# Optimization experiments

Measured on AMD Instinct MI355X. Metric: run time of the kernel, lower is better.

The kernel has to match this reference:

```python
import jax, jax.numpy as jnp
import numpy as np

N_HEAD = 16
T_THRESHOLD = 0.001


def setup_inputs() -> dict:
    key = jax.random.key(0)
    k_x, k_wa, k_ba, k_wp, k_bp = jax.random.split(key, 5)
    B, P, L, R = 8, 1024, 4, 256
    C = L * R  # n_embd = 1024
    s = 1.0 / np.sqrt(C)
    return {
        "x": jax.random.normal(k_x, (B, P, L, R), dtype=jnp.float32),
        "w_attn": jax.random.normal(k_wa, (C, 3 * C), dtype=jnp.float32) * s,
        "b_attn": jax.random.normal(k_ba, (3 * C,), dtype=jnp.float32) * 0.01,
        "w_proj": jax.random.normal(k_wp, (C, C), dtype=jnp.float32) * s,
        "b_proj": jax.random.normal(k_bp, (C,), dtype=jnp.float32) * 0.01,
    }


def reference(x, w_attn, b_attn, w_proj, b_proj):
    B, P, L, R = x.shape
    C = L * R
    H = N_HEAD
    hd = C // H
    xf = x.reshape(B, P, C)                      # (B, T, C)
    qkv = xf @ w_attn + b_attn                   # (B, T, 3C)
    q, k, v = jnp.split(qkv, 3, axis=-1)
    # (B, H, T, hd)
    q = q.reshape(B, P, H, hd).transpose(0, 2, 1, 3)
    k = k.reshape(B, P, H, hd).transpose(0, 2, 1, 3)
    v = v.reshape(B, P, H, hd).transpose(0, 2, 1, 3)
    att = jnp.einsum("bhqd,bhkd->bhqk", q, k) * (1.0 / np.sqrt(hd))
    att = jax.nn.softmax(att, axis=-1)
    att = jax.nn.relu(att - T_THRESHOLD)         # post-softmax thresholding
    y = jnp.einsum("bhqk,bhkd->bhqd", att, v)    # (B, H, T, hd)
    y = y.transpose(0, 2, 1, 3).reshape(B, P, C)
    y = y @ w_proj + b_proj
    return y.reshape(B, P, L, R)
```

## Files before the change

### kernel.cpp

```cpp
#include <hip/hip_runtime.h>


typedef _Float16 half8 __attribute__((ext_vector_type(8)));
typedef _Float16 half4_t __attribute__((ext_vector_type(4)));
typedef float floatx4 __attribute__((ext_vector_type(4)));

__device__ __forceinline__ void gl2lds16(const void* gsrc, void* lds) {
    __builtin_amdgcn_global_load_lds(
        (const __attribute__((address_space(1))) unsigned int*)gsrc,
        (__attribute__((address_space(3))) unsigned int*)lds,
        16, 0, 0);
}

__global__ __launch_bounds__(256) void prep(const float4* __restrict__ x4,
                                            _Float16* __restrict__ xh,
                                            const float* __restrict__ wa,
                                            _Float16* __restrict__ waT,
                                            const float* __restrict__ wp,
                                            _Float16* __restrict__ wpT) {
    __shared__ _Float16 t[64 * 65];
    int bid = blockIdx.x;
    if (bid < 4096) {
        int idx = bid * 256 + threadIdx.x;
#pragma unroll
        for (int i = idx; i < 2097152; i += 1048576) {
            float4 v = x4[i];
            half4_t h = { (_Float16)v.x, (_Float16)v.y, (_Float16)v.z, (_Float16)v.w };
            *(half4_t*)(xh + (size_t)i * 4) = h;
        }
    } else {
        int tt = bid - 4096;
        int by = tt & 15, bx = tt >> 4;
        const float* in = wa; _Float16* out = waT; int C = 3072;
        if (bx >= 48) { bx -= 48; in = wp; out = wpT; C = 1024; }
#pragma unroll
        for (int it = 0; it < 16; ++it) {
            int idx = it * 256 + threadIdx.x;
            int r = idx >> 6, c = idx & 63;
            t[c * 65 + r] = (_Float16)in[(size_t)(by * 64 + r) * C + bx * 64 + c];
        }
        __syncthreads();
#pragma unroll
        for (int it = 0; it < 16; ++it) {
            int idx = it * 256 + threadIdx.x;
            int rn = idx >> 6, ck = idx & 63;
            out[(size_t)(bx * 64 + rn) * 1024 + by * 64 + ck] = t[rn * 65 + ck];
        }
    }
}

#define GBAR __builtin_amdgcn_s_barrier()
#define WLGKM do { asm volatile("s_waitcnt lgkmcnt(0)" ::: "memory"); } while (0)
#define WVM2  do { asm volatile("s_waitcnt vmcnt(2)"   ::: "memory"); } while (0)
#define WVM4  do { asm volatile("s_waitcnt vmcnt(4)"   ::: "memory"); } while (0)
#define WVM0  do { asm volatile("s_waitcnt vmcnt(0)"   ::: "memory"); } while (0)


#define WLDA(buf, rg)                                                                         \
    do {                                                                                      \
        _Pragma("unroll") for (int i = 0; i < 4; ++i) {                                       \
            int r_ = wm * 128 + ((rg) * 4 + i) * 16 + l15;                                    \
            _Pragma("unroll") for (int kk = 0; kk < 2; ++kk)                                  \
                a[i][kk] = *(const half8*)(sA + (buf) * 32768 + r_ * 128 +                    \
                                           ((((kk << 2) + quad) ^ (r_ & 7)) << 4));           \
        }                                                                                     \
    } while (0)

#define WLDB(buf, cg, bb)                                                                     \
    do {                                                                                      \
        _Pragma("unroll") for (int j = 0; j < 2; ++j) {                                       \
            int r_ = wn * 64 + ((cg) * 2 + j) * 16 + l15;                                     \
            _Pragma("unroll") for (int kk = 0; kk < 2; ++kk)                                  \
                bb[j][kk] = *(const half8*)(sB + (buf) * 32768 + r_ * 128 +                   \
                                            ((((kk << 2) + quad) ^ (r_ & 7)) << 4));          \
        }                                                                                     \
    } while (0)

#define WMMA(rg, cg, bb)                                                                      \
    do {                                                                                      \
        __builtin_amdgcn_s_setprio(1);                                                        \
        _Pragma("unroll") for (int kk = 0; kk < 2; ++kk)                                      \
            _Pragma("unroll") for (int i = 0; i < 4; ++i)                                     \
                _Pragma("unroll") for (int j = 0; j < 2; ++j)                                  \
                    acc[(rg) * 4 + i][(cg) * 2 + j] = __builtin_amdgcn_mfma_f32_16x16x32_f16( \
                        a[i][kk], bb[j][kk], acc[(rg) * 4 + i][(cg) * 2 + j], 0, 0, 0);       \
        __builtin_amdgcn_s_setprio(0);                                                        \
    } while (0)

__global__ __launch_bounds__(512, 2) void gemm_qkv(const _Float16* __restrict__ A,
                                                   const _Float16* __restrict__ BT,
                                                   const float* __restrict__ bias,
                                                   _Float16* __restrict__ qno,
                                                   _Float16* __restrict__ kPo,
                                                   _Float16* __restrict__ vPo) {
    __shared__ __attribute__((aligned(16))) char lds[131072];
    char* sA = lds;
    char* sB = lds + 65536;
    int tid = threadIdx.x;
    int W = tid >> 6, lane = tid & 63, quad = lane >> 4, l15 = lane & 15;
    int wm = W >> 2, wn = W & 3;
    int flat = blockIdx.y * 12 + blockIdx.x;
    int swz = (flat & 7) * 48 + (flat >> 3);
    int m0 = (swz / 12) * 256, n0 = (swz % 12) * 256;

    auto stA = [&](int buf, int half, int k0) {
#pragma unroll
        for (int rnd = 0; rnd < 2; ++rnd) {
            int c = rnd * 512 + tid;
            int row = c >> 3;
            int q = (c & 7) ^ (row & 7);
            const _Float16* src = A + (size_t)(m0 + half * 128 + row) * 1024 + k0 + q * 8;
            int off = __builtin_amdgcn_readfirstlane(buf * 32768 + half * 16384 +
                                                     rnd * 8192 + (W << 10));
            gl2lds16(src, sA + off);
        }
    };
    auto stB = [&](int buf, int half, int k0) {
#pragma unroll
        for (int rnd = 0; rnd < 2; ++rnd) {
            int c = rnd * 512 + tid;
            int row = c >> 3;
            int q = (c & 7) ^ (row & 7);
            const _Float16* src = BT + (size_t)(n0 + half * 128 + row) * 1024 + k0 + q * 8;
            int off = __builtin_amdgcn_readfirstlane(buf * 32768 + half * 16384 +
                                                     rnd * 8192 + (W << 10));
            gl2lds16(src, sB + off);
        }
    };

    half8 a[4][2], b0[2][2], b1[2][2];
    floatx4 acc[8][4] = {};

    stA(0, 0, 0); stA(0, 1, 0);
    stB(0, 0, 0); stB(0, 1, 0);
    stB(1, 0, 64); stB(1, 1, 64);
    WVM4;
    GBAR;

#pragma unroll 1
    for (int t = 0; t < 16; t += 2) {
        int k1 = (t + 1) << 6;
        int k2 = ((t + 2) & 15) << 6;
        int k3 = ((t + 3) & 15) << 6;
        WLDA(0, 0); WLDB(0, 0, b0); stA(1, 0, k1);
        GBAR; WLGKM; WMMA(0, 0, b0); GBAR;
        WLDB(0, 1, b1); stA(1, 1, k1);
        GBAR; WLGKM; WMMA(0, 1, b1); GBAR;
        WLDA(0, 1); stB(0, 0, k2);
        GBAR; WLGKM; WMMA(1, 1, b1); GBAR;
        stB(0, 1, k2); WVM4;
        GBAR; WLGKM; WMMA(1, 0, b0); GBAR;
        WLDA(1, 0); WLDB(1, 0, b0); stA(0, 0, k2);
        GBAR; WLGKM; WMMA(0, 0, b0); GBAR;
        WLDB(1, 1, b1); stA(0, 1, k2);
        GBAR; WLGKM; WMMA(0, 1, b1); GBAR;
        WLDA(1, 1); stB(1, 0, k3);
        GBAR; WLGKM; WMMA(1, 1, b1); GBAR;
        stB(1, 1, k3); WVM4;
        GBAR; WLGKM; WMMA(1, 0, b0); GBAR;
    }

    WVM0;
    GBAR;
    int sec = n0 >> 10;
    int b = m0 >> 10;
    int tb = m0 & 1023;
#pragma unroll 1
    for (int p = 0; p < 2; ++p) {
        if (p) __syncthreads();
        if (sec == 2) {
            if ((wn >> 1) == p) {
#pragma unroll
                for (int cf = 0; cf < 4; ++cf) {
                    int lc = (wn & 1) * 64 + cf * 16 + l15;
                    float bv = bias[n0 + wn * 64 + cf * 16 + l15];
#pragma unroll
                    for (int rf = 0; rf < 8; ++rf) {
                        int m = wm * 128 + rf * 16 + quad * 4;
                        half4_t h4;
#pragma unroll
                        for (int r = 0; r < 4; ++r) h4[r] = (_Float16)(acc[rf][cf][r] + bv);
                        *(half4_t*)(lds + lc * 528 + m * 2) = h4;
                    }
                }
            }
            __syncthreads();
            int l15v = tid & 15;
            int moct = W * 4 + ((tid >> 4) & 3);
            int t = tb + moct * 8;
            int kbv = (t >> 5) & 31, quad_v = (t >> 3) & 3;
            int nbV = (n0 & 1023) + p * 128;
#pragma unroll
            for (int i = 0; i < 8; ++i) {
                int hh = i >> 2, cf = i & 3;
                int n = hh * 64 + cf * 16 + l15v;
                half8 v = *(const half8*)(lds + n * 528 + (moct << 4));
                int gcol = nbV + n;
                int h = gcol >> 6, d = gcol & 63;
                size_t chunk = (size_t)((b * 16 + h) * 32 + kbv) * 256 +
                               (d >> 4) * 64 + quad_v * 16 + (d & 15);
                *(half8*)(vPo + chunk * 8) = v;
            }
        } else {
            if ((wn >> 1) == p) {
#pragma unroll
                for (int cf = 0; cf < 4; ++cf) {
                    int lc = (wn & 1) * 64 + cf * 16 + l15;
                    float bv = bias[n0 + wn * 64 + cf * 16 + l15];
#pragma unroll
                    for (int rf = 0; rf < 8; ++rf) {
                        int m = wm * 128 + rf * 16 + quad * 4;
#pragma unroll
                        for (int r = 0; r < 4; ++r)
                            *(_Float16*)(lds + (m + r) * 272 + lc * 2) =
                                (_Float16)(acc[rf][cf][r] + bv);
                    }
                }
            }
            __syncthreads();
            int nb = (n0 & 1023) + p * 128;
            if (sec == 0) {
                int noct = tid & 15;
#pragma unroll
                for (int i = 0; i < 8; ++i) {
                    int m = i * 32 + (tid >> 4);
                    half8 v = *(const half8*)(lds + m * 272 + (noct << 4));
                    *(half8*)(qno + (size_t)(b * 1024 + tb + m) * 1024 + nb + noct * 8) = v;
                }
            } else {
                int l15k = tid & 15, noct = (tid >> 4) & 15;
#pragma unroll
                for (int i = 0; i < 8; ++i) {
                    int mb = i * 2 + (tid >> 8);
                    int m = mb * 16 + l15k;
                    half8 v = *(const half8*)(lds + m * 272 + (noct << 4));
                    int gcol = nb + noct * 8;
                    int h = gcol >> 6, d0 = gcol & 63;
                    int t = tb + m;
                    size_t chunk = (size_t)((b * 16 + h) * 64 + (t >> 4)) * 128 +
                                   (d0 >> 5) * 64 + ((d0 >> 3) & 3) * 16 + l15k;
                    *(half8*)(kPo + chunk * 8) = v;
                }
            }
        }
    }
}

#define LDA(buf, rg)                                                                          \
    do {                                                                                      \
        _Pragma("unroll") for (int i = 0; i < 2; ++i) {                                       \
            int r_ = wm * 64 + ((rg) * 2 + i) * 16 + l15;                                     \
            _Pragma("unroll") for (int kk = 0; kk < 2; ++kk)                                  \
                a[i][kk] = *(const half8*)(sA + (buf) * 32768 + r_ * 128 +                    \
                                           ((((kk << 2) + quad) ^ (r_ & 7)) << 4));           \
        }                                                                                     \
    } while (0)

#define LDB(buf, cg, bb)                                                                      \
    do {                                                                                      \
        _Pragma("unroll") for (int j = 0; j < 2; ++j) {                                       \
            int r_ = wn * 64 + ((cg) * 2 + j) * 16 + l15;                                     \
            _Pragma("unroll") for (int kk = 0; kk < 2; ++kk)                                  \
                bb[j][kk] = *(const half8*)(sB + (buf) * 16384 + r_ * 128 +                   \
                                            ((((kk << 2) + quad) ^ (r_ & 7)) << 4));          \
        }                                                                                     \
    } while (0)

#define MMA(rg, cg, bb)                                                                       \
    do {                                                                                      \
        __builtin_amdgcn_s_setprio(1);                                                        \
        _Pragma("unroll") for (int kk = 0; kk < 2; ++kk)                                      \
            _Pragma("unroll") for (int i = 0; i < 2; ++i)                                     \
                _Pragma("unroll") for (int j = 0; j < 2; ++j)                                  \
                    acc[(rg) * 2 + i][(cg) * 2 + j] = __builtin_amdgcn_mfma_f32_16x16x32_f16( \
                        a[i][kk], bb[j][kk], acc[(rg) * 2 + i][(cg) * 2 + j], 0, 0, 0);       \
        __builtin_amdgcn_s_setprio(0);                                                        \
    } while (0)

__global__ __launch_bounds__(512, 2) void gemm_proj(const _Float16* __restrict__ A,
                                                    const _Float16* __restrict__ BT,
                                                    const float* __restrict__ bias,
                                                    float* __restrict__ o0, int N) {
    __shared__ __attribute__((aligned(16))) char lds[98304];
    char* sA = lds;
    char* sB = lds + 65536;
    int tid = threadIdx.x;
    int W = tid >> 6, lane = tid & 63, quad = lane >> 4, l15 = lane & 15;
    int wm = W >> 1, wn = W & 1;
    int flat = blockIdx.y * 8 + blockIdx.x;
    int swz = (flat & 7) * 32 + (flat >> 3);
    int m0 = (swz >> 3) * 256, n0 = (swz & 7) * 128;

    auto stA = [&](int buf, int half, int k0) {
#pragma unroll
        for (int rnd = 0; rnd < 2; ++rnd) {
            int c = rnd * 512 + tid;
            int row = c >> 3;
            int q = (c & 7) ^ (row & 7);
            const _Float16* src = A + (size_t)(m0 + half * 128 + row) * 1024 + k0 + q * 8;
            int off = __builtin_amdgcn_readfirstlane(buf * 32768 + half * 16384 +
                                                     rnd * 8192 + (W << 10));
            gl2lds16(src, sA + off);
        }
    };
    auto stB = [&](int buf, int half, int k0) {
        int row = tid >> 3;
        int q = (tid & 7) ^ (row & 7);
        const _Float16* src = BT + (size_t)(n0 + half * 64 + row) * 1024 + k0 + q * 8;
        int off = __builtin_amdgcn_readfirstlane(buf * 16384 + half * 8192 + (W << 10));
        gl2lds16(src, sB + off);
    };

    half8 a[2][2], b0[2][2], b1[2][2];
    floatx4 acc[4][4] = {};

    stA(0, 0, 0); stA(0, 1, 0);
    stB(0, 0, 0); stB(0, 1, 0);
    stB(1, 0, 64); stB(1, 1, 64);
    WVM2;
    GBAR;

#pragma unroll 1
    for (int t = 0; t < 16; t += 2) {
        int k1 = (t + 1) << 6;
        int k2 = ((t + 2) & 15) << 6;
        int k3 = ((t + 3) & 15) << 6;
        LDA(0, 0); LDB(0, 0, b0); stA(1, 0, k1);
        GBAR; WLGKM; MMA(0, 0, b0); GBAR;
        LDB(0, 1, b1); stA(1, 1, k1);
        GBAR; WLGKM; MMA(0, 1, b1); GBAR;
        LDA(0, 1); stB(0, 0, k2);
        GBAR; WLGKM; MMA(1, 1, b1); GBAR;
        stB(0, 1, k2); WVM2;
        GBAR; WLGKM; MMA(1, 0, b0); GBAR;
        LDA(1, 0); LDB(1, 0, b0); stA(0, 0, k2);
        GBAR; WLGKM; MMA(0, 0, b0); GBAR;
        LDB(1, 1, b1); stA(0, 1, k2);
        GBAR; WLGKM; MMA(0, 1, b1); GBAR;
        LDA(1, 1); stB(1, 0, k3);
        GBAR; WLGKM; MMA(1, 1, b1); GBAR;
        stB(1, 1, k3); WVM2;
        GBAR; WLGKM; MMA(1, 0, b0); GBAR;
    }

#pragma unroll
    for (int cf = 0; cf < 4; ++cf) {
        int gn = n0 + wn * 64 + cf * 16 + l15;
        float bv = bias[gn];
#pragma unroll
        for (int rf = 0; rf < 4; ++rf) {
            int gmBase = m0 + wm * 64 + rf * 16 + quad * 4;
#pragma unroll
            for (int r = 0; r < 4; ++r)
                o0[(size_t)(gmBase + r) * N + gn] = acc[rf][cf][r] + bv;
        }
    }
}

__device__ __forceinline__ int esw(int row, int colByte) {
    return row * 2048 + (colByte ^ ((row & 7) << 4));
}

__global__ __launch_bounds__(512, 4) void attn(const _Float16* __restrict__ qn,
                                               const _Float16* __restrict__ kP,
                                               const _Float16* __restrict__ vP,
                                               _Float16* __restrict__ y) {
    __shared__ __attribute__((aligned(16))) _Float16 E[32 * 1024];
    __shared__ float lsum[8][32];
    char* Eb = (char*)E;
    int tid = threadIdx.x;
    int W = tid >> 6, lane = tid & 63, quad = lane >> 4, l15 = lane & 15;
    int flat = blockIdx.y * 32 + blockIdx.x;
    int swz = (flat & 7) * 512 + (flat >> 3);
    int qt = swz & 31, bh = swz >> 5;
    int b = bh >> 4, h = bh & 15;
    int q0 = qt * 32;

    half8 bq[2][2];
#pragma unroll
    for (int nf = 0; nf < 2; ++nf)
#pragma unroll
        for (int ks = 0; ks < 2; ++ks)
            bq[nf][ks] = *(const half8*)(qn + (size_t)(b * 1024 + q0 + nf * 16 + l15) * 1024 +
                                         h * 64 + ks * 32 + quad * 8);

    half8 ak[8][2];
#pragma unroll
    for (int mt = 0; mt < 8; ++mt) {
        const _Float16* kp = kP + ((size_t)(bh * 64 + W * 8 + mt) * 128 + lane) * 8;
        ak[mt][0] = *(const half8*)(kp);
        ak[mt][1] = *(const half8*)(kp + 512);
    }
    float lp0[2] = {0.f, 0.f}, lp1[2] = {0.f, 0.f};
#pragma unroll
    for (int mt = 0; mt < 8; ++mt) {
#pragma unroll
        for (int nf = 0; nf < 2; ++nf) {
            floatx4 s = {};
            s = __builtin_amdgcn_mfma_f32_16x16x32_f16(ak[mt][0], bq[nf][0], s, 0, 0, 0);
            s = __builtin_amdgcn_mfma_f32_16x16x32_f16(ak[mt][1], bq[nf][1], s, 0, 0, 0);
            half4_t h4;
            float esum0 = 0.f, esum1 = 0.f;
#pragma unroll
            for (int r = 0; r < 4; ++r) {
                float e = __builtin_amdgcn_exp2f(fminf(s[r] * 0.18033688f, 14.4269504f));
                if (r & 1) esum1 += e; else esum0 += e;
                h4[r] = (_Float16)e;
            }
            lp0[nf] += esum0;
            lp1[nf] += esum1;
            int q = nf * 16 + l15;
            int kbyte = (W * 128 + mt * 16 + quad * 4) * 2;
            *(half4_t*)(Eb + q * 2048 + (kbyte ^ ((q & 7) << 4))) = h4;
        }
    }
#pragma unroll
    for (int nf = 0; nf < 2; ++nf) {
        float lp = lp0[nf] + lp1[nf];
        lp += __shfl_xor(lp, 16);
        lp += __shfl_xor(lp, 32);
        if (lane < 16) lsum[W][nf * 16 + l15] = lp;
    }
    __syncthreads();

    half8 bv[4][4];
#pragma unroll
    for (int kt = 0; kt < 4; ++kt) {
        const _Float16* vbase = vP + ((size_t)(bh * 32 + (W * 4 + kt)) * 256 + lane) * 8;
#pragma unroll
        for (int cf = 0; cf < 4; ++cf)
            bv[kt][cf] = *(const half8*)(vbase + cf * 512);
    }
    half8 inv8[2], t8, z8;
#pragma unroll
    for (int j = 0; j < 8; ++j) { t8[j] = (_Float16)(-0.001f); z8[j] = (_Float16)0.f; }
#pragma unroll
    for (int rf = 0; rf < 2; ++rf) {
        float l = 0.f;
#pragma unroll
        for (int w = 0; w < 8; ++w) l += lsum[w][rf * 16 + l15];
        _Float16 invh = (_Float16)(1.0f / l);
#pragma unroll
        for (int j = 0; j < 8; ++j) inv8[rf][j] = invh;
    }

    floatx4 acc[2][4] = {};
#pragma unroll
    for (int kt = 0; kt < 4; ++kt) {
        int kk = W * 128 + kt * 32;
        half8 ap[2];
#pragma unroll
        for (int rf = 0; rf < 2; ++rf) {
            ap[rf] = *(const half8*)(Eb + esw(rf * 16 + l15, (kk + quad * 8) * 2));
            ap[rf] = ap[rf] * inv8[rf] + t8;
            ap[rf] = __builtin_elementwise_max(ap[rf], z8);
        }
#pragma unroll
        for (int rf = 0; rf < 2; ++rf)
#pragma unroll
            for (int cf = 0; cf < 4; ++cf)
                acc[rf][cf] = __builtin_amdgcn_mfma_f32_16x16x32_f16(ap[rf], bv[kt][cf], acc[rf][cf], 0, 0, 0);
    }

#pragma unroll
    for (int rf = 0; rf < 2; ++rf)
#pragma unroll
        for (int cf = 0; cf < 4; ++cf)
#pragma unroll
            for (int r = 0; r < 4; ++r) {
                int row = rf * 16 + quad * 4 + r;
                *(float*)(Eb + row * 2048 + W * 256 + (cf * 16 + l15) * 4) = acc[rf][cf][r];
            }
    __syncthreads();
    {
        int e4 = tid * 4;
        int r = e4 >> 6, c = e4 & 63;
        floatx4 s = {};
#pragma unroll
        for (int w = 0; w < 8; ++w)
            s += *(const floatx4*)(Eb + r * 2048 + w * 256 + c * 4);
        half4_t hv = { (_Float16)s[0], (_Float16)s[1], (_Float16)s[2], (_Float16)s[3] };
        *(half4_t*)(y + (size_t)(b * 1024 + q0 + r) * 1024 + h * 64 + c) = hv;
    }
}

extern "C" void kernel_launch(void* const* d_in, const int* in_sizes, int n_in,
                              void* d_out, int out_size, void* d_ws, size_t ws_size,
                              hipStream_t stream) {
    const float* x  = (const float*)d_in[0];
    const float* wa = (const float*)d_in[1];
    const float* ba = (const float*)d_in[2];
    const float* wp = (const float*)d_in[3];
    const float* bp = (const float*)d_in[4];
    float* out = (float*)d_out;

    char* ws = (char*)d_ws;
    _Float16* y   = (_Float16*)(ws);
    _Float16* qn  = (_Float16*)(ws + 16777216);
    _Float16* kP  = (_Float16*)(ws + 33554432);
    _Float16* vP  = (_Float16*)(ws + 50331648);
    _Float16* waT = (_Float16*)(ws + 67108864);
    _Float16* wpT = (_Float16*)(ws + 73400320);
    _Float16* xh  = (_Float16*)(ws + 75497472);

    prep<<<5120, 256, 0, stream>>>((const float4*)x, xh, wa, waT, wp, wpT);
    gemm_qkv<<<dim3(12, 32), 512, 0, stream>>>(xh, waT, ba, qn, kP, vP);
    attn<<<dim3(32, 128), 512, 0, stream>>>(qn, kP, vP, y);
    gemm_proj<<<dim3(8, 32), 512, 0, stream>>>(y, wpT, bp, out, 1024);
}
```

Baseline: 244.3 us.

## Switch attention to 32x32x16 MFMA and keep probabilities in registers

The attention kernel now uses 32x32x16 MFMA tiles instead of 16x16x32. The softmax probability tile stays in registers, repacked through cross-lane shuffles into the A-operand layout, where it used to round-trip through LDS. The QKV projection epilogue now writes K and V in the new packed layouts the 32x32 fragments need. V is loaded per step instead of all up front, and setprio hints are added around the MFMA groups. This cuts LDS traffic and MFMA instruction count, at the cost of extra shuffles and different register pressure.

```diff
diff --git a/kernel.cpp b/kernel.cpp
--- a/kernel.cpp
+++ b/kernel.cpp
@@ -4,12 +4,21 @@
 typedef _Float16 half8 __attribute__((ext_vector_type(8)));
 typedef _Float16 half4_t __attribute__((ext_vector_type(4)));
 typedef float floatx4 __attribute__((ext_vector_type(4)));
+typedef float floatx16 __attribute__((ext_vector_type(16)));
+typedef unsigned int uint4v __attribute__((ext_vector_type(4)));
 
 __device__ __forceinline__ void gl2lds16(const void* gsrc, void* lds) {
     __builtin_amdgcn_global_load_lds(
         (const __attribute__((address_space(1))) unsigned int*)gsrc,
         (__attribute__((address_space(3))) unsigned int*)lds,
         16, 0, 0);
+}
+
+__device__ __forceinline__ unsigned pkh(float a, float b) {
+    _Float16 ha = (_Float16)a, hb = (_Float16)b;
+    unsigned short ua = __builtin_bit_cast(unsigned short, ha);
+    unsigned short ub = __builtin_bit_cast(unsigned short, hb);
+    return (unsigned)ua | ((unsigned)ub << 16);
 }
 
 __global__ __launch_bounds__(256) void prep(const float4* __restrict__ x4,
@@ -54,7 +63,6 @@
 #define WVM2  do { asm volatile("s_waitcnt vmcnt(2)"   ::: "memory"); } while (0)
 #define WVM4  do { asm volatile("s_waitcnt vmcnt(4)"   ::: "memory"); } while (0)
 #define WVM0  do { asm volatile("s_waitcnt vmcnt(0)"   ::: "memory"); } while (0)
-
 
 #define WLDA(buf, rg)                                                                         \
     do {                                                                                      \
@@ -165,6 +173,7 @@
     int sec = n0 >> 10;
     int b = m0 >> 10;
     int tb = m0 & 1023;
+    int t31 = tid & 31, hi = (tid >> 5) & 1;
 #pragma unroll 1
     for (int p = 0; p < 2; ++p) {
         if (p) __syncthreads();
@@ -185,21 +194,16 @@
                 }
             }
             __syncthreads();
-            int l15v = tid & 15;
-            int moct = W * 4 + ((tid >> 4) & 3);
-            int t = tb + moct * 8;
-            int kbv = (t >> 5) & 31, quad_v = (t >> 3) & 3;
             int nbV = (n0 & 1023) + p * 128;
 #pragma unroll
             for (int i = 0; i < 8; ++i) {
-                int hh = i >> 2, cf = i & 3;
-                int n = hh * 64 + cf * 16 + l15v;
-                half8 v = *(const half8*)(lds + n * 528 + (moct << 4));
-                int gcol = nbV + n;
-                int h = gcol >> 6, d = gcol & 63;
-                size_t chunk = (size_t)((b * 16 + h) * 32 + kbv) * 256 +
-                               (d >> 4) * 64 + quad_v * 16 + (d & 15);
-                *(half8*)(vPo + chunk * 8) = v;
+                int g = W * 8 + i;
+                int h_loc = g >> 5, dh = (g >> 4) & 1, kcl = g & 15;
+                int lc = h_loc * 64 + dh * 32 + t31;
+                half8 v = *(const half8*)(lds + lc * 528 + kcl * 32 + hi * 16);
+                int hg = (nbV >> 6) + h_loc;
+                size_t cv = ((size_t)((b * 16 + hg) * 64 + (tb >> 4) + kcl) * 2 + dh) * 64 + lane;
+                *(half8*)(vPo + cv * 8) = v;
             }
         } else {
             if ((wn >> 1) == p) {
@@ -228,18 +232,16 @@
                     *(half8*)(qno + (size_t)(b * 1024 + tb + m) * 1024 + nb + noct * 8) = v;
                 }
             } else {
-                int l15k = tid & 15, noct = (tid >> 4) & 15;
 #pragma unroll
                 for (int i = 0; i < 8; ++i) {
-                    int mb = i * 2 + (tid >> 8);
-                    int m = mb * 16 + l15k;
-                    half8 v = *(const half8*)(lds + m * 272 + (noct << 4));
-                    int gcol = nb + noct * 8;
-                    int h = gcol >> 6, d0 = gcol & 63;
-                    int t = tb + m;
-                    size_t chunk = (size_t)((b * 16 + h) * 64 + (t >> 4)) * 128 +
-                                   (d0 >> 5) * 64 + ((d0 >> 3) & 3) * 16 + l15k;
-                    *(half8*)(kPo + chunk * 8) = v;
+                    int g = W * 8 + i;
+                    int h_loc = g >> 5, ks = (g >> 3) & 3, kbl = g & 7;
+                    int m = kbl * 32 + t31;
+                    int lc = h_loc * 64 + ks * 16 + hi * 8;
+                    half8 v = *(const half8*)(lds + m * 272 + ((lc >> 3) << 4));
+                    int hg = (nb >> 6) + h_loc;
+                    size_t ck = ((size_t)((b * 16 + hg) * 32 + (tb >> 5) + kbl) * 4 + ks) * 64 + lane;
+                    *(half8*)(kPo + ck * 8) = v;
                 }
             }
         }
@@ -357,120 +359,116 @@
     }
 }
 
-__device__ __forceinline__ int esw(int row, int colByte) {
-    return row * 2048 + (colByte ^ ((row & 7) << 4));
-}
-
 __global__ __launch_bounds__(512, 4) void attn(const _Float16* __restrict__ qn,
                                                const _Float16* __restrict__ kP,
                                                const _Float16* __restrict__ vP,
                                                _Float16* __restrict__ y) {
-    __shared__ __attribute__((aligned(16))) _Float16 E[32 * 1024];
+    __shared__ __attribute__((aligned(16))) char red[65536];
     __shared__ float lsum[8][32];
-    char* Eb = (char*)E;
     int tid = threadIdx.x;
-    int W = tid >> 6, lane = tid & 63, quad = lane >> 4, l15 = lane & 15;
+    int W = tid >> 6, lane = tid & 63;
+    int l31 = lane & 31, hi = lane >> 5;
     int flat = blockIdx.y * 32 + blockIdx.x;
     int swz = (flat & 7) * 512 + (flat >> 3);
     int qt = swz & 31, bh = swz >> 5;
     int b = bh >> 4, h = bh & 15;
     int q0 = qt * 32;
 
-    half8 bq[2][2];
-#pragma unroll
-    for (int nf = 0; nf < 2; ++nf)
-#pragma unroll
-        for (int ks = 0; ks < 2; ++ks)
-            bq[nf][ks] = *(const half8*)(qn + (size_t)(b * 1024 + q0 + nf * 16 + l15) * 1024 +
-                                         h * 64 + ks * 32 + quad * 8);
-
-    half8 ak[8][2];
-#pragma unroll
-    for (int mt = 0; mt < 8; ++mt) {
-        const _Float16* kp = kP + ((size_t)(bh * 64 + W * 8 + mt) * 128 + lane) * 8;
-        ak[mt][0] = *(const half8*)(kp);
-        ak[mt][1] = *(const half8*)(kp + 512);
-    }
-    float lp0[2] = {0.f, 0.f}, lp1[2] = {0.f, 0.f};
-#pragma unroll
-    for (int mt = 0; mt < 8; ++mt) {
-#pragma unroll
-        for (int nf = 0; nf < 2; ++nf) {
-            floatx4 s = {};
-            s = __builtin_amdgcn_mfma_f32_16x16x32_f16(ak[mt][0], bq[nf][0], s, 0, 0, 0);
-            s = __builtin_amdgcn_mfma_f32_16x16x32_f16(ak[mt][1], bq[nf][1], s, 0, 0, 0);
-            half4_t h4;
-            float esum0 = 0.f, esum1 = 0.f;
-#pragma unroll
-            for (int r = 0; r < 4; ++r) {
-                float e = __builtin_amdgcn_exp2f(fminf(s[r] * 0.18033688f, 14.4269504f));
-                if (r & 1) esum1 += e; else esum0 += e;
-                h4[r] = (_Float16)e;
-            }
-            lp0[nf] += esum0;
-            lp1[nf] += esum1;
-            int q = nf * 16 + l15;
-            int kbyte = (W * 128 + mt * 16 + quad * 4) * 2;
-            *(half4_t*)(Eb + q * 2048 + (kbyte ^ ((q & 7) << 4))) = h4;
-        }
-    }
-#pragma unroll
-    for (int nf = 0; nf < 2; ++nf) {
-        float lp = lp0[nf] + lp1[nf];
-        lp += __shfl_xor(lp, 16);
+    half8 bq[4];
+#pragma unroll
+    for (int ks = 0; ks < 4; ++ks)
+        bq[ks] = *(const half8*)(qn + (size_t)(b * 1024 + q0 + l31) * 1024 +
+                                 h * 64 + ks * 16 + hi * 8);
+
+    half8 pd[4][2];
+    float lp0 = 0.f, lp1 = 0.f;
+#pragma unroll
+    for (int kb = 0; kb < 4; ++kb) {
+        const _Float16* kpb = kP + ((size_t)((bh * 32 + W * 4 + kb) * 4) * 64 + lane) * 8;
+        half8 ak0 = *(const half8*)(kpb);
+        half8 ak1 = *(const half8*)(kpb + 512);
+        half8 ak2 = *(const half8*)(kpb + 1024);
+        half8 ak3 = *(const half8*)(kpb + 1536);
+        floatx16 s = {};
+        __builtin_amdgcn_s_setprio(1);
+        s = __builtin_amdgcn_mfma_f32_32x32x16_f16(ak0, bq[0], s, 0, 0, 0);
+        s = __builtin_amdgcn_mfma_f32_32x32x16_f16(ak1, bq[1], s, 0, 0, 0);
+        s = __builtin_amdgcn_mfma_f32_32x32x16_f16(ak2, bq[2], s, 0, 0, 0);
+        s = __builtin_amdgcn_mfma_f32_32x32x16_f16(ak3, bq[3], s, 0, 0, 0);
+        __builtin_amdgcn_s_setprio(0);
+        float e[16];
+#pragma unroll
+        for (int r = 0; r < 16; ++r)
+            e[r] = __builtin_amdgcn_exp2f(fminf(s[r] * 0.18033688f, 14.4269504f));
+        lp0 += ((e[0] + e[1]) + (e[2] + e[3])) + ((e[4] + e[5]) + (e[6] + e[7]));
+        lp1 += ((e[8] + e[9]) + (e[10] + e[11])) + ((e[12] + e[13]) + (e[14] + e[15]));
+#pragma unroll
+        for (int c = 0; c < 2; ++c) {
+            int o = c * 8;
+            unsigned P01 = pkh(e[o + 0], e[o + 1]);
+            unsigned P23 = pkh(e[o + 2], e[o + 3]);
+            unsigned P45 = pkh(e[o + 4], e[o + 5]);
+            unsigned P67 = pkh(e[o + 6], e[o + 7]);
+            unsigned P01p = (unsigned)__shfl_xor((int)P45, 32);
+            unsigned P45p = (unsigned)__shfl_xor((int)P01, 32);
+            unsigned P23p = (unsigned)__shfl_xor((int)P67, 32);
+            unsigned P67p = (unsigned)__shfl_xor((int)P23, 32);
+            uint4v F;
+            F[0] = hi ? P01p : P01;
+            F[1] = hi ? P23p : P23;
+            F[2] = hi ? P45 : P45p;
+            F[3] = hi ? P67 : P67p;
+            pd[kb][c] = __builtin_bit_cast(half8, F);
+        }
+    }
+    {
+        float lp = lp0 + lp1;
         lp += __shfl_xor(lp, 32);
-        if (lane < 16) lsum[W][nf * 16 + l15] = lp;
+        if (lane < 32) lsum[W][l31] = lp;
     }
     __syncthreads();
 
-    half8 bv[4][4];
-#pragma unroll
-    for (int kt = 0; kt < 4; ++kt) {
-        const _Float16* vbase = vP + ((size_t)(bh * 32 + (W * 4 + kt)) * 256 + lane) * 8;
-#pragma unroll
-        for (int cf = 0; cf < 4; ++cf)
-            bv[kt][cf] = *(const half8*)(vbase + cf * 512);
-    }
-    half8 inv8[2], t8, z8;
+    half8 inv8, t8, z8;
 #pragma unroll
     for (int j = 0; j < 8; ++j) { t8[j] = (_Float16)(-0.001f); z8[j] = (_Float16)0.f; }
-#pragma unroll
-    for (int rf = 0; rf < 2; ++rf) {
+    {
         float l = 0.f;
 #pragma unroll
-        for (int w = 0; w < 8; ++w) l += lsum[w][rf * 16 + l15];
+        for (int w = 0; w < 8; ++w) l += lsum[w][l31];
         _Float16 invh = (_Float16)(1.0f / l);
 #pragma unroll
-        for (int j = 0; j < 8; ++j) inv8[rf][j] = invh;
-    }
-
-    floatx4 acc[2][4] = {};
-#pragma unroll
-    for (int kt = 0; kt < 4; ++kt) {
-        int kk = W * 128 + kt * 32;
-        half8 ap[2];
-#pragma unroll
-        for (int rf = 0; rf < 2; ++rf) {
-            ap[rf] = *(const half8*)(Eb + esw(rf * 16 + l15, (kk + quad * 8) * 2));
-            ap[rf] = ap[rf] * inv8[rf] + t8;
-            ap[rf] = __builtin_elementwise_max(ap[rf], z8);
-        }
-#pragma unroll
-        for (int rf = 0; rf < 2; ++rf)
-#pragma unroll
-            for (int cf = 0; cf < 4; ++cf)
-                acc[rf][cf] = __builtin_amdgcn_mfma_f32_16x16x32_f16(ap[rf], bv[kt][cf], acc[rf][cf], 0, 0, 0);
-    }
-
-#pragma unroll
-    for (int rf = 0; rf < 2; ++rf)
-#pragma unroll
-        for (int cf = 0; cf < 4; ++cf)
-#pragma unroll
-            for (int r = 0; r < 4; ++r) {
-                int row = rf * 16 + quad * 4 + r;
-                *(float*)(Eb + row * 2048 + W * 256 + (cf * 16 + l15) * 4) = acc[rf][cf][r];
-            }
+        for (int j = 0; j < 8; ++j) inv8[j] = invh;
+    }
+#pragma unroll
+    for (int kb = 0; kb < 4; ++kb)
+#pragma unroll
+        for (int c = 0; c < 2; ++c) {
+            pd[kb][c] = pd[kb][c] * inv8 + t8;
+            pd[kb][c] = __builtin_elementwise_max(pd[kb][c], z8);
+        }
+
+    floatx16 acc[2] = {};
+#pragma unroll
+    for (int kb = 0; kb < 4; ++kb)
+#pragma unroll
+        for (int c = 0; c < 2; ++c) {
+            int kc = (W * 4 + kb) * 2 + c;
+            const _Float16* vpb = vP + ((size_t)((bh * 64 + kc) * 2) * 64 + lane) * 8;
+            half8 bv0 = *(const half8*)(vpb);
+            half8 bv1 = *(const half8*)(vpb + 512);
+            __builtin_amdgcn_s_setprio(1);
+            acc[0] = __builtin_amdgcn_mfma_f32_32x32x16_f16(pd[kb][c], bv0, acc[0], 0, 0, 0);
+            acc[1] = __builtin_amdgcn_mfma_f32_32x32x16_f16(pd[kb][c], bv1, acc[1], 0, 0, 0);
+            __builtin_amdgcn_s_setprio(0);
+        }
+
+#pragma unroll
+    for (int dh = 0; dh < 2; ++dh)
+#pragma unroll
+        for (int r = 0; r < 16; ++r) {
+            int q = (r & 3) + 8 * (r >> 2) + 4 * hi;
+            *(float*)(red + q * 2048 + W * 256 + (dh * 32 + l31) * 4) = acc[dh][r];
+        }
     __syncthreads();
     {
         int e4 = tid * 4;
@@ -478,7 +476,7 @@
         floatx4 s = {};
 #pragma unroll
         for (int w = 0; w < 8; ++w)
-            s += *(const floatx4*)(Eb + r * 2048 + w * 256 + c * 4);
+            s += *(const floatx4*)(red + r * 2048 + w * 256 + c * 4);
         half4_t hv = { (_Float16)s[0], (_Float16)s[1], (_Float16)s[2], (_Float16)s[3] };
         *(half4_t*)(y + (size_t)(b * 1024 + q0 + r) * 1024 + h * 64 + c) = hv;
     }
```

New measurement: 266.0 us. 8.9% more time.
